# Kernel tuning notes

Measured on AMD Instinct MI355X. Metric: run time of the kernel, lower is better.

## Reference

```python
import jax, jax.numpy as jnp
import numpy as np

FOCAL_ALPHA = 0.25
FOCAL_GAMMA = 2.0
IOU_POS_THRESH = 0.5


def setup_inputs() -> dict:
    A, G, C = 262144, 256, 80
    key = jax.random.key(0)
    k = jax.random.split(key, 8)
    # anchors: random boxes with centers in [0,1024], sizes in [16,128]
    actr = jax.random.uniform(k[0], (A, 2), minval=0.0, maxval=1024.0)
    awh = jax.random.uniform(k[1], (A, 2), minval=16.0, maxval=128.0)
    anchors = jnp.concatenate([actr - 0.5 * awh, actr + 0.5 * awh], axis=1)
    # ground-truth boxes: sizes in [32,256]
    gctr = jax.random.uniform(k[2], (G, 2), minval=0.0, maxval=1024.0)
    gwh = jax.random.uniform(k[3], (G, 2), minval=32.0, maxval=256.0)
    gt_boxes = jnp.concatenate([gctr - 0.5 * gwh, gctr + 0.5 * gwh], axis=1)
    cls_logits = jax.random.normal(k[4], (A, C), dtype=jnp.float32)
    # small deltas so exp(delta * width) in this module's decode stays finite
    bbox_reg = jax.random.normal(k[5], (A, 4), dtype=jnp.float32) * 0.02
    centerness = jax.random.normal(k[6], (A,), dtype=jnp.float32)
    gt_labels = jax.random.randint(k[7], (G,), 0, C, dtype=jnp.int32)
    return {"anchors": anchors, "cls_logits": cls_logits, "bbox_reg": bbox_reg,
            "centerness": centerness, "gt_boxes": gt_boxes, "gt_labels": gt_labels}


def _compute_loss(anchors, cls_logits, bbox_reg, centerness, gt_boxes, gt_labels):
    A, C = cls_logits.shape
    f32 = cls_logits.dtype
    # ---- box_iou: [A, G] pairwise IoU ----
    area_a = (anchors[:, 2] - anchors[:, 0]) * (anchors[:, 3] - anchors[:, 1])
    area_g = (gt_boxes[:, 2] - gt_boxes[:, 0]) * (gt_boxes[:, 3] - gt_boxes[:, 1])
    lt = jnp.maximum(anchors[:, None, :2], gt_boxes[None, :, :2])
    rb = jnp.minimum(anchors[:, None, 2:], gt_boxes[None, :, 2:])
    wh = jnp.maximum(rb - lt, 0.0)
    inter = wh[..., 0] * wh[..., 1]
    iou = inter / (area_a[:, None] + area_g[None, :] - inter)
    max_iou = iou.max(axis=1)
    midx = iou.argmax(axis=1)
    pos = max_iou > IOU_POS_THRESH
    posf = pos.astype(f32)
    npos = posf.sum()
    denom = jnp.maximum(npos, 1.0)
    mboxes = gt_boxes[midx]            # [A,4] matched GT box per anchor
    mlabels = gt_labels[midx]          # [A]
    # ---- focal loss over ALL anchors (targets = -1 for negatives) ----
    cls_t = jnp.where(pos, mlabels, -1)
    logp = jax.nn.log_softmax(cls_logits, axis=-1)
    # torch gathers class index; -1 wraps to last class (python-style indexing)
    ce = -jnp.take_along_axis(logp, (cls_t % C)[:, None], axis=1)[:, 0]
    p = jnp.exp(-ce)
    fl = (1.0 - p) ** FOCAL_GAMMA * ce
    af = jnp.where(cls_t == 1, FOCAL_ALPHA, 1.0 - FOCAL_ALPHA)
    cls_loss = (af * fl).mean()
    # ---- decode boxes (module's unusual parameterization: exp(delta*width)*width) ----
    w = anchors[:, 2] - anchors[:, 0]
    h = anchors[:, 3] - anchors[:, 1]
    cx = anchors[:, 0] + 0.5 * w
    cy = anchors[:, 1] + 0.5 * h
    pcx = cx + bbox_reg[:, 0] * w
    pcy = cy + bbox_reg[:, 1] * h
    pw = jnp.exp(bbox_reg[:, 2] * w) * w
    ph = jnp.exp(bbox_reg[:, 3] * h) * h
    pred = jnp.stack([pcx - 0.5 * pw, pcy - 0.5 * ph, pcx + 0.5 * pw, pcy + 0.5 * ph], axis=1)
    # ---- paired GIoU (diag of generalized_box_iou(pred, matched)) ----
    lt2 = jnp.maximum(pred[:, :2], mboxes[:, :2])
    rb2 = jnp.minimum(pred[:, 2:], mboxes[:, 2:])
    wh2 = jnp.maximum(rb2 - lt2, 0.0)
    inter2 = wh2[:, 0] * wh2[:, 1]
    area_p = (pred[:, 2] - pred[:, 0]) * (pred[:, 3] - pred[:, 1])
    area_m = (mboxes[:, 2] - mboxes[:, 0]) * (mboxes[:, 3] - mboxes[:, 1])
    union = area_p + area_m - inter2
    iou2 = inter2 / union
    el = jnp.minimum(pred[:, :2], mboxes[:, :2])
    er = jnp.maximum(pred[:, 2:], mboxes[:, 2:])
    ewh = jnp.maximum(er - el, 0.0)
    earea = ewh[:, 0] * ewh[:, 1]
    giou = iou2 - (earea - union) / earea
    reg_loss = 1.0 - (posf * giou).sum() / denom
    # ---- centerness targets + BCE-with-logits over positives ----
    lr = mboxes[:, jnp.array([0, 2])] - anchors[:, jnp.array([0, 2])]
    tb = mboxes[:, jnp.array([1, 3])] - anchors[:, jnp.array([1, 3])]
    lrmax = lr.max(axis=1)
    tbmax = tb.max(axis=1)
    r_lr = jnp.maximum(lr.min(axis=1) / jnp.where(lrmax == 0, 1.0, lrmax), 0.0)
    r_tb = jnp.maximum(tb.min(axis=1) / jnp.where(tbmax == 0, 1.0, tbmax), 0.0)
    ctr_t = jnp.sqrt(jnp.maximum(r_lr * r_tb, 1e-12))
    bce = jnp.logaddexp(0.0, centerness) - centerness * ctr_t
    ctr_loss = (posf * bce).sum() / denom
    # original skips the level entirely when there are no positives
    has = (npos > 0).astype(f32)
    cls_loss = cls_loss * has
    reg_loss = reg_loss * has
    ctr_loss = ctr_loss * has
    total = cls_loss + reg_loss + ctr_loss
    return total, cls_loss, reg_loss, ctr_loss


def reference(anchors, cls_logits, bbox_reg, centerness, gt_boxes, gt_labels):
    return _compute_loss(anchors, cls_logits, bbox_reg, centerness, gt_boxes, gt_labels)
```

## Files before the change

kernel.cpp:

```cpp
#include <hip/hip_runtime.h>
#include <math.h>

#define BLOCK 256
#define C_CLS 80
#define G_MAX 256
#define NCELL1 32
#define NCELLS (NCELL1 * NCELL1)
#define CAP 96
#define NBKT 256

static __device__ inline float frcp(float x) { return __builtin_amdgcn_rcpf(x); }

static __device__ inline int cell_of(float4 ab) {
    const float cx = 0.5f * (ab.x + ab.z);
    const float cy = 0.5f * (ab.y + ab.w);
    int ix = (int)(cx * (1.0f / 32.0f));
    int iy = (int)(cy * (1.0f / 32.0f));
    ix = ix < 0 ? 0 : (ix > NCELL1 - 1 ? NCELL1 - 1 : ix);
    iy = iy < 0 ? 0 : (iy > NCELL1 - 1 ? NCELL1 - 1 : iy);
    return iy * NCELL1 + ix;
}


__global__ __launch_bounds__(256) void k_build(
    const float4* __restrict__ gt, const int* __restrict__ gl,
    float* __restrict__ bsums, int* __restrict__ cnts,
    float4* __restrict__ boxes, int* __restrict__ labs, int G)
{
    __shared__ int s_wcnt[4];
    const int cell = blockIdx.x;
    const int ix = cell & (NCELL1 - 1), iy = cell >> 5;
    const float Dx1 = 32.0f * ix - 64.0f, Dx2 = 32.0f * ix + 96.0f;
    const float Dy1 = 32.0f * iy - 64.0f, Dy2 = 32.0f * iy + 96.0f;

    const int tid = threadIdx.x, wid = tid >> 6, lane = tid & 63;
    if (cell < NBKT && tid < 4) bsums[cell * 4 + tid] = 0.0f;

    bool keep = false;
    float4 g = make_float4(0.f, 0.f, 0.f, 0.f);
    int lb = 0;
    if (tid < G) {
        g = gt[tid];
        const float area_g = (g.z - g.x) * (g.w - g.y);
        const float iwW = fmaxf(fminf(g.z, Dx2) - fmaxf(g.x, Dx1), 0.0f);
        const float ihW = fmaxf(fminf(g.w, Dy2) - fmaxf(g.y, Dy1), 0.0f);
        keep = (iwW * ihW > 0.4999f * area_g) && (area_g < 32800.0f);
        lb = gl[tid];
    }
    const unsigned long long mk = __ballot(keep);
    if (lane == 0) s_wcnt[wid] = __popcll(mk);
    __syncthreads();
    int prefix = 0;
    for (int w = 0; w < wid; ++w) prefix += s_wcnt[w];
    if (keep) {
        const int p = prefix + __popcll(mk & ((1ull << lane) - 1ull));
        if (p < CAP) {
            boxes[(size_t)cell * CAP + p] = g;
            labs[(size_t)cell * CAP + p] = lb;
        }
    }
    const int tot = s_wcnt[0] + s_wcnt[1] + s_wcnt[2] + s_wcnt[3];
    if (tid == 0) cnts[cell] = (tot > CAP) ? (1 << 30) : tot;
}

__global__ __launch_bounds__(BLOCK) void k_main(
    const float* __restrict__ anchors, const float* __restrict__ cls_logits,
    const float* __restrict__ bbox_reg, const float* __restrict__ centerness,
    const float* __restrict__ gt_boxes, const int* __restrict__ gt_labels,
    const int* __restrict__ cnts, const float4* __restrict__ boxes,
    const int* __restrict__ labs,
    float* __restrict__ bsums, int A, int G)
{
    const int tid = threadIdx.x;
    const int a = blockIdx.x * BLOCK + tid;
    const bool valid = a < A;
    const int ar = valid ? a : 0;

    const float4* __restrict__ row4 =
        reinterpret_cast<const float4*>(cls_logits + (size_t)ar * C_CLS);
    float4 rr[C_CLS / 4];
    #pragma unroll
    for (int k = 0; k < C_CLS / 4; ++k) rr[k] = row4[k];
    #pragma unroll
    for (int k = 0; k < C_CLS / 4; ++k)
        asm volatile("" :: "v"(rr[k].x), "v"(rr[k].y), "v"(rr[k].z), "v"(rr[k].w));

    const float4 ab = reinterpret_cast<const float4*>(anchors)[ar];
    const float area_a = (ab.z - ab.x) * (ab.w - ab.y);

    const int cell = cell_of(ab);
    const int cnt = valid ? cnts[cell] : 0;
    const bool big = cnt > CAP;
    const int c2 = big ? 0 : cnt;

    const float4* __restrict__ bl = boxes + (size_t)cell * CAP;
    float best = -1.0f;
    int bestk = 0, bidx = 0;
    for (int j = 0; j < c2; ++j) {
        const float4 g = bl[j];
        const float ga = (g.z - g.x) * (g.w - g.y);
        const float lx = fmaxf(ab.x, g.x);
        const float ly = fmaxf(ab.y, g.y);
        const float rx = fminf(ab.z, g.z);
        const float ry = fminf(ab.w, g.w);
        const float iw = fmaxf(rx - lx, 0.0f);
        const float ih = fmaxf(ry - ly, 0.0f);
        const float inter = iw * ih;
        const float iou = inter * frcp(area_a + ga - inter);
        if (iou > best) { best = iou; bestk = j; }
    }

    if (__ballot(big) != 0ull) {
        if (big) {
            best = -1.0f; bidx = 0;
            for (int j = 0; j < G; ++j) {
                const float4 g = reinterpret_cast<const float4*>(gt_boxes)[j];
                const float ga = (g.z - g.x) * (g.w - g.y);
                const float lx = fmaxf(ab.x, g.x);
                const float ly = fmaxf(ab.y, g.y);
                const float rx = fminf(ab.z, g.z);
                const float ry = fminf(ab.w, g.w);
                const float iw = fmaxf(rx - lx, 0.0f);
                const float ih = fmaxf(ry - ly, 0.0f);
                const float inter = iw * ih;
                const float iou = inter * frcp(area_a + ga - inter);
                if (iou > best) { best = iou; bidx = j; }
            }
        }
    }

    float c_affl = 0.f, c_pos = 0.f, c_giou = 0.f, c_bce = 0.f;

    if (valid) {
        const bool pos = best > 0.5f;
        int lab = -1;
        float4 mb = make_float4(0.f, 0.f, 0.f, 0.f);
        if (pos) {
            if (big) { mb = reinterpret_cast<const float4*>(gt_boxes)[bidx]; lab = gt_labels[bidx]; }
            else     { mb = bl[bestk]; lab = labs[(size_t)cell * CAP + bestk]; }
        }

        float m = -3.4e38f;
        #pragma unroll
        for (int k = 0; k < C_CLS / 4; ++k) {
            const float4 v = rr[k];
            m = fmaxf(m, fmaxf(fmaxf(v.x, v.y), fmaxf(v.z, v.w)));
        }
        float s = 0.0f;
        #pragma unroll
        for (int k = 0; k < C_CLS / 4; ++k) {
            const float4 v = rr[k];
            s += __expf(v.x - m) + __expf(v.y - m)
               + __expf(v.z - m) + __expf(v.w - m);
        }
        const float v79 = rr[C_CLS / 4 - 1].w;
        const float lse = m + __logf(s);
        const float l_idx = pos ? cls_logits[(size_t)a * C_CLS + lab] : v79;
        const float ce = lse - l_idx;
        const float p  = __expf(-ce);
        const float om = 1.0f - p;
        const float fl = om * om * ce;
        const float af = (pos && lab == 1) ? 0.25f : 0.75f;
        c_affl = af * fl;

        if (pos) {
            const float w  = ab.z - ab.x;
            const float h  = ab.w - ab.y;
            const float cx = ab.x + 0.5f * w;
            const float cy = ab.y + 0.5f * h;
            const float4 t = reinterpret_cast<const float4*>(bbox_reg)[a];
            const float pcx = cx + t.x * w;
            const float pcy = cy + t.y * h;
            const float pw  = __expf(t.z * w) * w;
            const float ph  = __expf(t.w * h) * h;
            const float p0 = pcx - 0.5f * pw;
            const float p1 = pcy - 0.5f * ph;
            const float p2 = pcx + 0.5f * pw;
            const float p3 = pcy + 0.5f * ph;

            const float lx2 = fmaxf(p0, mb.x);
            const float ly2 = fmaxf(p1, mb.y);
            const float rx2 = fminf(p2, mb.z);
            const float ry2 = fminf(p3, mb.w);
            const float iw2 = fmaxf(rx2 - lx2, 0.0f);
            const float ih2 = fmaxf(ry2 - ly2, 0.0f);
            const float inter2 = iw2 * ih2;
            const float area_p = (p2 - p0) * (p3 - p1);
            const float area_m = (mb.z - mb.x) * (mb.w - mb.y);
            const float uni = area_p + area_m - inter2;
            const float iou2 = inter2 * frcp(uni);
            const float elx = fminf(p0, mb.x);
            const float ely = fminf(p1, mb.y);
            const float erx = fmaxf(p2, mb.z);
            const float ery = fmaxf(p3, mb.w);
            const float ew = fmaxf(erx - elx, 0.0f);
            const float eh = fmaxf(ery - ely, 0.0f);
            const float earea = ew * eh;
            const float giou = iou2 - (earea - uni) * frcp(earea);
            c_giou = giou;

            const float lr0 = mb.x - ab.x;
            const float lr1 = mb.z - ab.z;
            const float tb0 = mb.y - ab.y;
            const float tb1 = mb.w - ab.w;
            const float lrmax = fmaxf(lr0, lr1);
            const float lrmin = fminf(lr0, lr1);
            const float tbmax = fmaxf(tb0, tb1);
            const float tbmin = fminf(tb0, tb1);
            const float r_lr = fmaxf(lrmin * frcp(lrmax == 0.0f ? 1.0f : lrmax), 0.0f);
            const float r_tb = fmaxf(tbmin * frcp(tbmax == 0.0f ? 1.0f : tbmax), 0.0f);
            const float ctr_t = sqrtf(fmaxf(r_lr * r_tb, 1e-12f));
            const float c = centerness[a];
            const float bce = fmaxf(c, 0.0f) + log1pf(__expf(-fabsf(c))) - c * ctr_t;
            c_bce = bce;
            c_pos = 1.0f;
        }
    }

    __shared__ float red[4][BLOCK / 64];
    float vals[4] = { c_affl, c_pos, c_giou, c_bce };
    #pragma unroll
    for (int i = 0; i < 4; ++i) {
        float v = vals[i];
        #pragma unroll
        for (int off = 32; off > 0; off >>= 1) v += __shfl_down(v, off, 64);
        if ((tid & 63) == 0) red[i][tid >> 6] = v;
    }
    __syncthreads();
    if (tid < 4) {
        float v = 0.f;
        #pragma unroll
        for (int wv = 0; wv < BLOCK / 64; ++wv) v += red[tid][wv];
        atomicAdd(&bsums[(blockIdx.x & (NBKT - 1)) * 4 + tid], v);
    }
}

__global__ __launch_bounds__(BLOCK) void detloss_fallback(
    const float* __restrict__ anchors, const float* __restrict__ cls_logits,
    const float* __restrict__ bbox_reg, const float* __restrict__ centerness,
    const float* __restrict__ gt_boxes, const int* __restrict__ gt_labels,
    float* __restrict__ bsums, int A, int G)
{
    __shared__ float4 s_gt[G_MAX];
    __shared__ float  s_ga[G_MAX];
    __shared__ int    s_gl[G_MAX];
    const int tid = threadIdx.x;
    for (int j = tid; j < G; j += BLOCK) {
        float4 g = reinterpret_cast<const float4*>(gt_boxes)[j];
        s_gt[j] = g;
        s_ga[j] = (g.z - g.x) * (g.w - g.y);
        s_gl[j] = gt_labels[j];
    }
    __syncthreads();
    const int a = blockIdx.x * BLOCK + tid;
    float c_affl = 0.f, c_pos = 0.f, c_giou = 0.f, c_bce = 0.f;
    if (a < A) {
        const float4 ab = reinterpret_cast<const float4*>(anchors)[a];
        const float area_a = (ab.z - ab.x) * (ab.w - ab.y);
        float best = -1.0f; int bidx = 0;
        for (int j = 0; j < G; ++j) {
            const float4 g = s_gt[j];
            const float lx = fmaxf(ab.x, g.x), ly = fmaxf(ab.y, g.y);
            const float rx = fminf(ab.z, g.z), ry = fminf(ab.w, g.w);
            const float iw = fmaxf(rx - lx, 0.0f), ih = fmaxf(ry - ly, 0.0f);
            const float inter = iw * ih;
            const float iou = inter * frcp(area_a + s_ga[j] - inter);
            if (iou > best) { best = iou; bidx = j; }
        }
        const bool pos = best > 0.5f;
        const float posf = pos ? 1.0f : 0.0f;
        const float4 mb = s_gt[bidx];
        const int mlab = s_gl[bidx];
        const float4* row4 = reinterpret_cast<const float4*>(cls_logits + (size_t)a * C_CLS);
        float m = -3.4e38f, s = 0.0f, v79 = 0.0f;
        #pragma unroll
        for (int k = 0; k < C_CLS / 4; ++k) {
            const float4 v = row4[k];
            const float m4 = fmaxf(fmaxf(v.x, v.y), fmaxf(v.z, v.w));
            const float mn = fmaxf(m, m4);
            s = s * __expf(m - mn) + __expf(v.x - mn) + __expf(v.y - mn)
              + __expf(v.z - mn) + __expf(v.w - mn);
            m = mn;
            if (k == C_CLS / 4 - 1) v79 = v.w;
        }
        const float lse = m + __logf(s);
        const float l_idx = pos ? cls_logits[(size_t)a * C_CLS + mlab] : v79;
        const float ce = lse - l_idx;
        const float p = __expf(-ce);
        const float om = 1.0f - p;
        const float fl = om * om * ce;
        const float af = (pos && mlab == 1) ? 0.25f : 0.75f;
        c_affl = af * fl;
        const float w = ab.z - ab.x, h = ab.w - ab.y;
        const float cx = ab.x + 0.5f * w, cy = ab.y + 0.5f * h;
        const float4 t = reinterpret_cast<const float4*>(bbox_reg)[a];
        const float pcx = cx + t.x * w, pcy = cy + t.y * h;
        const float pw = __expf(t.z * w) * w, ph = __expf(t.w * h) * h;
        const float p0 = pcx - 0.5f * pw, p1 = pcy - 0.5f * ph;
        const float p2 = pcx + 0.5f * pw, p3 = pcy + 0.5f * ph;
        const float lx2 = fmaxf(p0, mb.x), ly2 = fmaxf(p1, mb.y);
        const float rx2 = fminf(p2, mb.z), ry2 = fminf(p3, mb.w);
        const float iw2 = fmaxf(rx2 - lx2, 0.0f), ih2 = fmaxf(ry2 - ly2, 0.0f);
        const float inter2 = iw2 * ih2;
        const float area_p = (p2 - p0) * (p3 - p1);
        const float area_m = (mb.z - mb.x) * (mb.w - mb.y);
        const float uni = area_p + area_m - inter2;
        const float iou2 = inter2 * frcp(uni);
        const float elx = fminf(p0, mb.x), ely = fminf(p1, mb.y);
        const float erx = fmaxf(p2, mb.z), ery = fmaxf(p3, mb.w);
        const float ew = fmaxf(erx - elx, 0.0f), eh = fmaxf(ery - ely, 0.0f);
        const float earea = ew * eh;
        const float giou = iou2 - (earea - uni) * frcp(earea);
        c_giou = posf * giou;
        const float lr0 = mb.x - ab.x, lr1 = mb.z - ab.z;
        const float tb0 = mb.y - ab.y, tb1 = mb.w - ab.w;
        const float lrmax = fmaxf(lr0, lr1), lrmin = fminf(lr0, lr1);
        const float tbmax = fmaxf(tb0, tb1), tbmin = fminf(tb0, tb1);
        const float r_lr = fmaxf(lrmin * frcp(lrmax == 0.0f ? 1.0f : lrmax), 0.0f);
        const float r_tb = fmaxf(tbmin * frcp(tbmax == 0.0f ? 1.0f : tbmax), 0.0f);
        const float ctr_t = sqrtf(fmaxf(r_lr * r_tb, 1e-12f));
        const float c = centerness[a];
        const float bce = fmaxf(c, 0.0f) + log1pf(__expf(-fabsf(c))) - c * ctr_t;
        c_bce = posf * bce;
        c_pos = posf;
    }
    __shared__ float red[4][BLOCK / 64];
    float vals[4] = { c_affl, c_pos, c_giou, c_bce };
    #pragma unroll
    for (int i = 0; i < 4; ++i) {
        float v = vals[i];
        #pragma unroll
        for (int off = 32; off > 0; off >>= 1) v += __shfl_down(v, off, 64);
        if ((tid & 63) == 0) red[i][tid >> 6] = v;
    }
    __syncthreads();
    if (tid < 4) {
        float v = 0.f;
        #pragma unroll
        for (int w = 0; w < BLOCK / 64; ++w) v += red[tid][w];
        atomicAdd(&bsums[(blockIdx.x & (NBKT - 1)) * 4 + tid], v);
    }
}

__global__ __launch_bounds__(NBKT) void detloss_final(
    const float* __restrict__ bsums, float* __restrict__ out, int A)
{
    const int t = threadIdx.x;
    float4 v = reinterpret_cast<const float4*>(bsums)[t];
    #pragma unroll
    for (int off = 32; off > 0; off >>= 1) {
        v.x += __shfl_down(v.x, off, 64);
        v.y += __shfl_down(v.y, off, 64);
        v.z += __shfl_down(v.z, off, 64);
        v.w += __shfl_down(v.w, off, 64);
    }
    __shared__ float4 r[NBKT / 64];
    if ((t & 63) == 0) r[t >> 6] = v;
    __syncthreads();
    if (t == 0) {
        float s_affl = 0.f, npos = 0.f, sgiou = 0.f, sbce = 0.f;
        #pragma unroll
        for (int w = 0; w < NBKT / 64; ++w) {
            s_affl += r[w].x; npos += r[w].y; sgiou += r[w].z; sbce += r[w].w;
        }
        float cls = s_affl / (float)A;
        const float denom = fmaxf(npos, 1.0f);
        float reg = 1.0f - sgiou / denom;
        float ctr = sbce / denom;
        const float has = (npos > 0.0f) ? 1.0f : 0.0f;
        cls *= has; reg *= has; ctr *= has;
        out[0] = cls + reg + ctr;
        out[1] = cls;
        out[2] = reg;
        out[3] = ctr;
    }
}

extern "C" void kernel_launch(void* const* d_in, const int* in_sizes, int n_in,
                              void* d_out, int out_size, void* d_ws, size_t ws_size,
                              hipStream_t stream) {
    const float* anchors    = (const float*)d_in[0];
    const float* cls_logits = (const float*)d_in[1];
    const float* bbox_reg   = (const float*)d_in[2];
    const float* centerness = (const float*)d_in[3];
    const float* gt_boxes   = (const float*)d_in[4];
    const int*   gt_labels  = (const int*)d_in[5];
    const int A = in_sizes[0] / 4;
    const int G = in_sizes[4] / 4;

    float* bsums = (float*)d_ws;
    const int grid = (A + BLOCK - 1) / BLOCK;

    const size_t need = (size_t)(4 * NBKT + NCELLS + (size_t)NCELLS * CAP * 4
                                 + (size_t)NCELLS * CAP) * 4;

    if (ws_size >= need && G <= 256) {
        int*    cnts  = (int*)d_ws + 4 * NBKT;
        float4* boxes = (float4*)((float*)d_ws + 4 * NBKT + NCELLS);
        int*    labs  = (int*)((float*)d_ws + 4 * NBKT + NCELLS + (size_t)NCELLS * CAP * 4);

        k_build<<<NCELLS, 256, 0, stream>>>((const float4*)gt_boxes, gt_labels,
                                            bsums, cnts, boxes, labs, G);
        k_main<<<grid, BLOCK, 0, stream>>>(anchors, cls_logits, bbox_reg,
                                           centerness, gt_boxes, gt_labels,
                                           cnts, boxes, labs, bsums, A, G);
    } else {
        const int Gc = G > G_MAX ? G_MAX : G;
        (void)hipMemsetAsync(bsums, 0, 4 * NBKT * sizeof(float), stream);
        detloss_fallback<<<grid, BLOCK, 0, stream>>>(anchors, cls_logits, bbox_reg,
                                                     centerness, gt_boxes, gt_labels,
                                                     bsums, A, Gc);
    }
    detloss_final<<<1, NBKT, 0, stream>>>(bsums, (float*)d_out, A);
}
```

Measured before the change: 35.39 us.

## Stage logits through LDS with coalesced loads and split rows across half-waves

The per-thread 320-byte row loads of class logits are replaced with wave-cooperative coalesced float4 loads into a padded shared-memory stage. Two lanes share each row's log-sum-exp and combine the halves with cross-half shuffles. Each wave now handles two passes of 32 anchors instead of one anchor per lane. This targets the uncoalesced global access pattern and the large register footprint. In exchange it duplicates the IoU matching work across both half-waves, leaves half the lanes idle in the loss tail, and adds LDS traffic.

Result: slower. 39.50 us (+11.6%).

```diff
diff --git a/kernel.cpp b/kernel.cpp
--- a/kernel.cpp
+++ b/kernel.cpp
@@ -8,6 +8,7 @@
 #define NCELLS (NCELL1 * NCELL1)
 #define CAP 96
 #define NBKT 256
+#define LSTRIDE 84
 
 static __device__ inline float frcp(float x) { return __builtin_amdgcn_rcpf(x); }
 
@@ -64,156 +65,177 @@
 }
 
 __global__ __launch_bounds__(BLOCK) void k_main(
-    const float* __restrict__ anchors, const float* __restrict__ cls_logits,
-    const float* __restrict__ bbox_reg, const float* __restrict__ centerness,
-    const float* __restrict__ gt_boxes, const int* __restrict__ gt_labels,
+    const float4* __restrict__ anchors4, const float* __restrict__ cls_logits,
+    const float4* __restrict__ bbox_reg4, const float* __restrict__ centerness,
+    const float4* __restrict__ gt4, const int* __restrict__ gl,
     const int* __restrict__ cnts, const float4* __restrict__ boxes,
     const int* __restrict__ labs,
     float* __restrict__ bsums, int A, int G)
 {
+    __shared__ float stage[4][32 * LSTRIDE];
     const int tid = threadIdx.x;
-    const int a = blockIdx.x * BLOCK + tid;
-    const bool valid = a < A;
-    const int ar = valid ? a : 0;
-
-    const float4* __restrict__ row4 =
-        reinterpret_cast<const float4*>(cls_logits + (size_t)ar * C_CLS);
-    float4 rr[C_CLS / 4];
+    const int wv = tid >> 6, lane = tid & 63;
+    const int r = lane & 31, h = lane >> 5;
+    float* __restrict__ st = stage[wv];
+
+    const long blockBase = (long)blockIdx.x * BLOCK;
+    const size_t fmaxidx = (size_t)A * (C_CLS / 4) - 1;
+
+    float c_affl = 0.f, c_pos = 0.f, c_giou = 0.f, c_bce = 0.f;
+
     #pragma unroll
-    for (int k = 0; k < C_CLS / 4; ++k) rr[k] = row4[k];
-    #pragma unroll
-    for (int k = 0; k < C_CLS / 4; ++k)
-        asm volatile("" :: "v"(rr[k].x), "v"(rr[k].y), "v"(rr[k].z), "v"(rr[k].w));
-
-    const float4 ab = reinterpret_cast<const float4*>(anchors)[ar];
-    const float area_a = (ab.z - ab.x) * (ab.w - ab.y);
-
-    const int cell = cell_of(ab);
-    const int cnt = valid ? cnts[cell] : 0;
-    const bool big = cnt > CAP;
-    const int c2 = big ? 0 : cnt;
-
-    const float4* __restrict__ bl = boxes + (size_t)cell * CAP;
-    float best = -1.0f;
-    int bestk = 0, bidx = 0;
-    for (int j = 0; j < c2; ++j) {
-        const float4 g = bl[j];
-        const float ga = (g.z - g.x) * (g.w - g.y);
-        const float lx = fmaxf(ab.x, g.x);
-        const float ly = fmaxf(ab.y, g.y);
-        const float rx = fminf(ab.z, g.z);
-        const float ry = fminf(ab.w, g.w);
-        const float iw = fmaxf(rx - lx, 0.0f);
-        const float ih = fmaxf(ry - ly, 0.0f);
-        const float inter = iw * ih;
-        const float iou = inter * frcp(area_a + ga - inter);
-        if (iou > best) { best = iou; bestk = j; }
-    }
-
-    if (__ballot(big) != 0ull) {
-        if (big) {
-            best = -1.0f; bidx = 0;
-            for (int j = 0; j < G; ++j) {
-                const float4 g = reinterpret_cast<const float4*>(gt_boxes)[j];
-                const float ga = (g.z - g.x) * (g.w - g.y);
-                const float lx = fmaxf(ab.x, g.x);
-                const float ly = fmaxf(ab.y, g.y);
-                const float rx = fminf(ab.z, g.z);
-                const float ry = fminf(ab.w, g.w);
-                const float iw = fmaxf(rx - lx, 0.0f);
-                const float ih = fmaxf(ry - ly, 0.0f);
-                const float inter = iw * ih;
-                const float iou = inter * frcp(area_a + ga - inter);
-                if (iou > best) { best = iou; bidx = j; }
+    for (int p = 0; p < 2; ++p) {
+        const long rowSet = blockBase + wv * 64 + p * 32;
+        const size_t fbase = (size_t)rowSet * (C_CLS / 4);
+
+        #pragma unroll
+        for (int k = 0; k < 10; ++k) {
+            const int fl = lane + 64 * k;
+            size_t f = fbase + fl;
+            f = f > fmaxidx ? fmaxidx : f;
+            const float4 v = reinterpret_cast<const float4*>(cls_logits)[f];
+            const int rr_ = fl / 20, cc = fl % 20;
+            *reinterpret_cast<float4*>(&st[rr_ * LSTRIDE + cc * 4]) = v;
+        }
+
+        const int row = (int)(rowSet + r);
+        const bool valid = row < A;
+        const int ar = valid ? row : 0;
+
+        const float* __restrict__ myb = &st[r * LSTRIDE + h * 40];
+        float4 hv[10];
+        #pragma unroll
+        for (int k = 0; k < 10; ++k)
+            hv[k] = *reinterpret_cast<const float4*>(&myb[4 * k]);
+        float lm = -3.4e38f;
+        #pragma unroll
+        for (int k = 0; k < 10; ++k) {
+            const float4 v = hv[k];
+            lm = fmaxf(lm, fmaxf(fmaxf(v.x, v.y), fmaxf(v.z, v.w)));
+        }
+        const float m = fmaxf(lm, __shfl_xor(lm, 32, 64));
+        float ls = 0.0f;
+        #pragma unroll
+        for (int k = 0; k < 10; ++k) {
+            const float4 v = hv[k];
+            ls += __expf(v.x - m) + __expf(v.y - m)
+                + __expf(v.z - m) + __expf(v.w - m);
+        }
+        const float s = ls + __shfl_xor(ls, 32, 64);
+        const float lse = m + __logf(s);
+        const float l_neg = st[r * LSTRIDE + 79];
+
+        const float4 ab = anchors4[ar];
+        const float area_a = (ab.z - ab.x) * (ab.w - ab.y);
+        const int cell = cell_of(ab);
+        const int cnt = valid ? cnts[cell] : 0;
+        const bool big = cnt > CAP;
+        const int c2 = big ? 0 : cnt;
+
+        const float4* __restrict__ bl = boxes + (size_t)cell * CAP;
+        float best = -1.0f;
+        int bestk = 0, bidx = 0;
+        for (int j = 0; j < c2; ++j) {
+            const float4 g = bl[j];
+            const float ga = (g.z - g.x) * (g.w - g.y);
+            const float lx = fmaxf(ab.x, g.x);
+            const float ly = fmaxf(ab.y, g.y);
+            const float rx = fminf(ab.z, g.z);
+            const float ry = fminf(ab.w, g.w);
+            const float iw = fmaxf(rx - lx, 0.0f);
+            const float ih = fmaxf(ry - ly, 0.0f);
+            const float inter = iw * ih;
+            const float iou = inter * frcp(area_a + ga - inter);
+            if (iou > best) { best = iou; bestk = j; }
+        }
+        if (__ballot(big) != 0ull) {
+            if (big) {
+                best = -1.0f; bidx = 0;
+                for (int j = 0; j < G; ++j) {
+                    const float4 g = gt4[j];
+                    const float ga = (g.z - g.x) * (g.w - g.y);
+                    const float lx = fmaxf(ab.x, g.x);
+                    const float ly = fmaxf(ab.y, g.y);
+                    const float rx = fminf(ab.z, g.z);
+                    const float ry = fminf(ab.w, g.w);
+                    const float iw = fmaxf(rx - lx, 0.0f);
+                    const float ih = fmaxf(ry - ly, 0.0f);
+                    const float inter = iw * ih;
+                    const float iou = inter * frcp(area_a + ga - inter);
+                    if (iou > best) { best = iou; bidx = j; }
+                }
             }
         }
-    }
-
-    float c_affl = 0.f, c_pos = 0.f, c_giou = 0.f, c_bce = 0.f;
-
-    if (valid) {
-        const bool pos = best > 0.5f;
-        int lab = -1;
-        float4 mb = make_float4(0.f, 0.f, 0.f, 0.f);
-        if (pos) {
-            if (big) { mb = reinterpret_cast<const float4*>(gt_boxes)[bidx]; lab = gt_labels[bidx]; }
-            else     { mb = bl[bestk]; lab = labs[(size_t)cell * CAP + bestk]; }
-        }
-
-        float m = -3.4e38f;
-        #pragma unroll
-        for (int k = 0; k < C_CLS / 4; ++k) {
-            const float4 v = rr[k];
-            m = fmaxf(m, fmaxf(fmaxf(v.x, v.y), fmaxf(v.z, v.w)));
-        }
-        float s = 0.0f;
-        #pragma unroll
-        for (int k = 0; k < C_CLS / 4; ++k) {
-            const float4 v = rr[k];
-            s += __expf(v.x - m) + __expf(v.y - m)
-               + __expf(v.z - m) + __expf(v.w - m);
-        }
-        const float v79 = rr[C_CLS / 4 - 1].w;
-        const float lse = m + __logf(s);
-        const float l_idx = pos ? cls_logits[(size_t)a * C_CLS + lab] : v79;
-        const float ce = lse - l_idx;
-        const float p  = __expf(-ce);
-        const float om = 1.0f - p;
-        const float fl = om * om * ce;
-        const float af = (pos && lab == 1) ? 0.25f : 0.75f;
-        c_affl = af * fl;
-
-        if (pos) {
-            const float w  = ab.z - ab.x;
-            const float h  = ab.w - ab.y;
-            const float cx = ab.x + 0.5f * w;
-            const float cy = ab.y + 0.5f * h;
-            const float4 t = reinterpret_cast<const float4*>(bbox_reg)[a];
-            const float pcx = cx + t.x * w;
-            const float pcy = cy + t.y * h;
-            const float pw  = __expf(t.z * w) * w;
-            const float ph  = __expf(t.w * h) * h;
-            const float p0 = pcx - 0.5f * pw;
-            const float p1 = pcy - 0.5f * ph;
-            const float p2 = pcx + 0.5f * pw;
-            const float p3 = pcy + 0.5f * ph;
-
-            const float lx2 = fmaxf(p0, mb.x);
-            const float ly2 = fmaxf(p1, mb.y);
-            const float rx2 = fminf(p2, mb.z);
-            const float ry2 = fminf(p3, mb.w);
-            const float iw2 = fmaxf(rx2 - lx2, 0.0f);
-            const float ih2 = fmaxf(ry2 - ly2, 0.0f);
-            const float inter2 = iw2 * ih2;
-            const float area_p = (p2 - p0) * (p3 - p1);
-            const float area_m = (mb.z - mb.x) * (mb.w - mb.y);
-            const float uni = area_p + area_m - inter2;
-            const float iou2 = inter2 * frcp(uni);
-            const float elx = fminf(p0, mb.x);
-            const float ely = fminf(p1, mb.y);
-            const float erx = fmaxf(p2, mb.z);
-            const float ery = fmaxf(p3, mb.w);
-            const float ew = fmaxf(erx - elx, 0.0f);
-            const float eh = fmaxf(ery - ely, 0.0f);
-            const float earea = ew * eh;
-            const float giou = iou2 - (earea - uni) * frcp(earea);
-            c_giou = giou;
-
-            const float lr0 = mb.x - ab.x;
-            const float lr1 = mb.z - ab.z;
-            const float tb0 = mb.y - ab.y;
-            const float tb1 = mb.w - ab.w;
-            const float lrmax = fmaxf(lr0, lr1);
-            const float lrmin = fminf(lr0, lr1);
-            const float tbmax = fmaxf(tb0, tb1);
-            const float tbmin = fminf(tb0, tb1);
-            const float r_lr = fmaxf(lrmin * frcp(lrmax == 0.0f ? 1.0f : lrmax), 0.0f);
-            const float r_tb = fmaxf(tbmin * frcp(tbmax == 0.0f ? 1.0f : tbmax), 0.0f);
-            const float ctr_t = sqrtf(fmaxf(r_lr * r_tb, 1e-12f));
-            const float c = centerness[a];
-            const float bce = fmaxf(c, 0.0f) + log1pf(__expf(-fabsf(c))) - c * ctr_t;
-            c_bce = bce;
-            c_pos = 1.0f;
+
+        if (h == 0 && valid) {
+            const bool pos = best > 0.5f;
+            int lab = -1;
+            float l_idx = l_neg;
+            float4 mb = make_float4(0.f, 0.f, 0.f, 0.f);
+            if (pos) {
+                if (big) { mb = gt4[bidx]; lab = gl[bidx]; }
+                else     { mb = bl[bestk]; lab = labs[(size_t)cell * CAP + bestk]; }
+                l_idx = cls_logits[(size_t)row * C_CLS + lab];
+            }
+            const float ce = lse - l_idx;
+            const float pr = __expf(-ce);
+            const float om = 1.0f - pr;
+            const float fl2 = om * om * ce;
+            const float af = (pos && lab == 1) ? 0.25f : 0.75f;
+            c_affl += af * fl2;
+
+            if (pos) {
+                const float w  = ab.z - ab.x;
+                const float hh = ab.w - ab.y;
+                const float cx = ab.x + 0.5f * w;
+                const float cy = ab.y + 0.5f * hh;
+                const float4 t = bbox_reg4[row];
+                const float pcx = cx + t.x * w;
+                const float pcy = cy + t.y * hh;
+                const float pw  = __expf(t.z * w) * w;
+                const float ph  = __expf(t.w * hh) * hh;
+                const float p0 = pcx - 0.5f * pw;
+                const float p1 = pcy - 0.5f * ph;
+                const float p2 = pcx + 0.5f * pw;
+                const float p3 = pcy + 0.5f * ph;
+
+                const float lx2 = fmaxf(p0, mb.x);
+                const float ly2 = fmaxf(p1, mb.y);
+                const float rx2 = fminf(p2, mb.z);
+                const float ry2 = fminf(p3, mb.w);
+                const float iw2 = fmaxf(rx2 - lx2, 0.0f);
+                const float ih2 = fmaxf(ry2 - ly2, 0.0f);
+                const float inter2 = iw2 * ih2;
+                const float area_p = (p2 - p0) * (p3 - p1);
+                const float area_m = (mb.z - mb.x) * (mb.w - mb.y);
+                const float uni = area_p + area_m - inter2;
+                const float iou2 = inter2 * frcp(uni);
+                const float elx = fminf(p0, mb.x);
+                const float ely = fminf(p1, mb.y);
+                const float erx = fmaxf(p2, mb.z);
+                const float ery = fmaxf(p3, mb.w);
+                const float ew = fmaxf(erx - elx, 0.0f);
+                const float eh = fmaxf(ery - ely, 0.0f);
+                const float earea = ew * eh;
+                const float giou = iou2 - (earea - uni) * frcp(earea);
+                c_giou += giou;
+
+                const float lr0 = mb.x - ab.x;
+                const float lr1 = mb.z - ab.z;
+                const float tb0 = mb.y - ab.y;
+                const float tb1 = mb.w - ab.w;
+                const float lrmax = fmaxf(lr0, lr1);
+                const float lrmin = fminf(lr0, lr1);
+                const float tbmax = fmaxf(tb0, tb1);
+                const float tbmin = fminf(tb0, tb1);
+                const float r_lr = fmaxf(lrmin * frcp(lrmax == 0.0f ? 1.0f : lrmax), 0.0f);
+                const float r_tb = fmaxf(tbmin * frcp(tbmax == 0.0f ? 1.0f : tbmax), 0.0f);
+                const float ctr_t = sqrtf(fmaxf(r_lr * r_tb, 1e-12f));
+                const float cc = centerness[row];
+                const float bce = fmaxf(cc, 0.0f) + log1pf(__expf(-fabsf(cc))) - cc * ctr_t;
+                c_bce += bce;
+                c_pos += 1.0f;
+            }
         }
     }
 
@@ -224,13 +246,13 @@
         float v = vals[i];
         #pragma unroll
         for (int off = 32; off > 0; off >>= 1) v += __shfl_down(v, off, 64);
-        if ((tid & 63) == 0) red[i][tid >> 6] = v;
+        if (lane == 0) red[i][wv] = v;
     }
     __syncthreads();
     if (tid < 4) {
         float v = 0.f;
         #pragma unroll
-        for (int wv = 0; wv < BLOCK / 64; ++wv) v += red[tid][wv];
+        for (int w = 0; w < BLOCK / 64; ++w) v += red[tid][w];
         atomicAdd(&bsums[(blockIdx.x & (NBKT - 1)) * 4 + tid], v);
     }
 }
@@ -401,8 +423,9 @@
 
         k_build<<<NCELLS, 256, 0, stream>>>((const float4*)gt_boxes, gt_labels,
                                             bsums, cnts, boxes, labs, G);
-        k_main<<<grid, BLOCK, 0, stream>>>(anchors, cls_logits, bbox_reg,
-                                           centerness, gt_boxes, gt_labels,
+        k_main<<<grid, BLOCK, 0, stream>>>((const float4*)anchors, cls_logits,
+                                           (const float4*)bbox_reg, centerness,
+                                           (const float4*)gt_boxes, gt_labels,
                                            cnts, boxes, labs, bsums, A, G);
     } else {
         const int Gc = G > G_MAX ? G_MAX : G;
```
